# Performance work log

Hardware: AMD Instinct MI355X
Metric: run time of the kernel (lower is better)

## Reference

```python
import jax, jax.numpy as jnp
import numpy as np

LMAX = 4
S2_DIM = (LMAX + 1) ** 2                                  # 25: s2 irreps, mul 1 per l
SO3_DIM = sum((2 * l + 1) ** 2 for l in range(LMAX + 1))  # 165: so3 irreps, mul 2l+1 per l
B = 2048
F_S2, F_SO3 = 1, 16
N_S2_KERNEL = 48      # s2_healpix_grid(rec_level=1)
N_SO3_KERNEL = 192    # so3_near_identity_grid()
N_ACT_GRID = 4000     # SO3Activation resolution=10, aspect_ratio=2 -> 20x10x20, flattened
N_EVAL = 4608         # so3_healpix_grid(rec_level=2): 192 pixels x 24 gamma


def setup_inputs() -> dict:
    ks = jax.random.split(jax.random.key(0), 7)
    return {
        "x": jax.random.normal(ks[0], (B, F_S2, S2_DIM), jnp.float32),
        "w_s2": jax.random.normal(ks[1], (F_S2, F_SO3, N_S2_KERNEL), jnp.float32),
        "Y": jax.random.normal(ks[2], (N_S2_KERNEL, S2_DIM), jnp.float32),
        "w_so3": jax.random.normal(ks[3], (F_SO3, 1, N_SO3_KERNEL), jnp.float32),
        "D_kernel": jax.random.normal(ks[4], (N_SO3_KERNEL, SO3_DIM), jnp.float32),
        "D_act": jax.random.normal(ks[5], (N_ACT_GRID, SO3_DIM), jnp.float32),
        "eval_wigners": jax.random.normal(ks[6], (SO3_DIM, N_EVAL), jnp.float32) / np.sqrt(SO3_DIM),
    }


def _s2_to_so3_linear(x, psi):
    # e3nn o3.Linear(s2_irreps -> so3_irreps, f_in, f_out, external weights)
    # x:   [B, f_in, 25]  (mul 1 per degree l)
    # psi: [f_in, f_out, 25] ; column l^2+j is the weight to output-multiplicity j of degree l
    f_in, f_out = psi.shape[0], psi.shape[1]
    out, s = [], 0
    for l in range(LMAX + 1):
        d = 2 * l + 1
        x_l = x[..., s:s + d]                       # [B, f_in, d]
        p_l = psi[..., s:s + d]                     # [f_in, f_out, d] (j = out-mul idx)
        o = jnp.einsum('bxm,xyj->byjm', x_l, p_l) / np.sqrt(f_in)
        out.append(o.reshape(x.shape[0], f_out, d * d))
        s += d
    return jnp.concatenate(out, axis=-1)            # [B, f_out, 165]


def _so3_to_so3_linear(x, psi):
    # e3nn o3.Linear(so3_irreps -> so3_irreps, f_in, f_out, external weights)
    # x:   [B, f_in, 165] ; psi: [f_in, f_out, 165]
    f_in, f_out = psi.shape[0], psi.shape[1]
    out, s = [], 0
    for l in range(LMAX + 1):
        d = 2 * l + 1
        x_l = x[..., s:s + d * d].reshape(x.shape[0], f_in, d, d)   # [B,f_in,u,m]
        p_l = psi[..., s:s + d * d].reshape(f_in, f_out, d, d)      # [f_in,f_out,u,v]
        o = jnp.einsum('bxum,xyuv->byvm', x_l, p_l) / np.sqrt(f_in * d)
        out.append(o.reshape(x.shape[0], f_out, d * d))
        s += d * d
    return jnp.concatenate(out, axis=-1)            # [B, f_out, 165]


def _forward(x, w_s2, Y, w_so3, D_kernel, D_act, eval_wigners):
    # --- S2Convolution: kernel = SH-transform of grid weights, then irrep-wise linear
    psi1 = jnp.einsum('ni,xyn->xyi', Y, w_s2) / np.sqrt(N_S2_KERNEL)     # [1,16,25]
    h = _s2_to_so3_linear(x, psi1)                                        # [B,16,165]
    # --- SO3Activation: Fourier -> SO(3) grid -> relu -> Fourier
    g = jnp.einsum('bfi,gi->bfg', h, D_act) / np.sqrt(SO3_DIM)            # [B,16,4000]
    g = jax.nn.relu(g)
    h = jnp.einsum('bfg,gi->bfi', g, D_act) * (np.sqrt(SO3_DIM) / N_ACT_GRID)
    # --- SO3Convolution
    psi2 = jnp.einsum('ni,xyn->xyi', D_kernel, w_so3) / np.sqrt(N_SO3_KERNEL)  # [16,1,165]
    harmonics = _so3_to_so3_linear(h, psi2)                               # [B,1,165]
    # --- compute_probabilities: matmul with eval Wigner-D basis + softmax over grid
    probs = jax.nn.softmax(jnp.einsum('bfi,ie->be', harmonics, eval_wigners), axis=1)  # [B,4608]
    # --- top-k masking: zero out everything below the 5th-highest prob of sample 0
    fifth = jax.lax.top_k(probs, 5)[0][0, 4]
    probs = jnp.where(probs < fifth, 0.0, probs)
    return harmonics, probs


def reference(x, w_s2, Y, w_so3, D_kernel, D_act, eval_wigners):
    return _forward(x, w_s2, Y, w_so3, D_kernel, D_act, eval_wigners)
```

## Files before the change

kernel.cpp:

```cpp
#include <hip/hip_runtime.h>

typedef short bf16x8 __attribute__((ext_vector_type(8)));
typedef float f32x16 __attribute__((ext_vector_type(16)));
typedef int   i32x4  __attribute__((ext_vector_type(4)));

#define INV_SQRT165 0.07784989441615349f
#define FINAL_SCALE 0.0032113081446662823f
#define ZERO16 ((f32x16){0.f,0.f,0.f,0.f,0.f,0.f,0.f,0.f,0.f,0.f,0.f,0.f,0.f,0.f,0.f,0.f})

__device__ __forceinline__ unsigned short f2bf(float f) {
  unsigned int u = __builtin_bit_cast(unsigned int, f);
  unsigned int r = (u + 0x7FFFu + ((u >> 16) & 1u)) >> 16;
  return (unsigned short)r;
}
__device__ __forceinline__ float bf2f(unsigned short h) {
  unsigned int u = ((unsigned int)h) << 16;
  return __builtin_bit_cast(float, u);
}
__device__ __forceinline__ unsigned int pack_bf2(float lo, float hi) {
  return ((unsigned int)f2bf(hi) << 16) | (unsigned int)f2bf(lo);
}

__device__ __forceinline__ void gl_lds16(const void* g, void* l) {
  __builtin_amdgcn_global_load_lds(
      (const __attribute__((address_space(1))) unsigned int*)(unsigned long long)g,
      (__attribute__((address_space(3))) unsigned int*)(unsigned int)(unsigned long long)l,
      16, 0, 0);
}

__device__ __forceinline__ void decode_i(int i, int& lv, int& rel) {
  if (i < 1)       { lv = 0; rel = i; }
  else if (i < 10) { lv = 1; rel = i - 1; }
  else if (i < 35) { lv = 2; rel = i - 10; }
  else if (i < 84) { lv = 3; rel = i - 35; }
  else             { lv = 4; rel = i - 84; }
}
__device__ __forceinline__ int divq(int rel, int lv) {
  const int mag[5] = {32768, 10923, 6554, 4682, 3641};
  return (rel * mag[lv]) >> 15;
}

__global__ void psi_k(const float* __restrict__ Y, const float* __restrict__ w_s2,
                      const float* __restrict__ Dk, const float* __restrict__ w_so3,
                      float* __restrict__ psi1, float* __restrict__ psi2) {
  int bx = blockIdx.x;
  if (bx < 2) {
    int t = bx * 256 + threadIdx.x;
    if (t >= 400) return;
    int y = t / 25, i = t % 25;
    float s = 0.f;
    for (int n = 0; n < 48; n++) s += Y[n * 25 + i] * w_s2[y * 48 + n];
    psi1[t] = s * 0.14433756729740643f;
  } else {
    int t = (bx - 2) * 256 + threadIdx.x;
    if (t >= 2640) return;
    int ch = t / 165, i = t % 165;
    float s = 0.f;
    for (int n = 0; n < 192; n++) s += Dk[n * 165 + i] * w_so3[ch * 192 + n];
    psi2[t] = s * 0.07216878364870323f;
  }
}

__global__ __launch_bounds__(256) void prep_k(const float* __restrict__ Da,
                                              const float* __restrict__ ew,
                                              const float* __restrict__ psi1,
                                              unsigned short* __restrict__ e1pre,
                                              unsigned short* __restrict__ d2pre,
                                              unsigned short* __restrict__ ewpre) {
  __shared__ __align__(16) unsigned short lds[13824];
  const int tid = threadIdx.x;
  const int l = tid & 63, hl = l >> 5, ln = l & 31;
  if (blockIdx.x < 128) {
    const int ci = blockIdx.x, g0 = ci * 32;
    float* psi1L = (float*)(lds + 6464);
    for (int e = tid; e < 6400; e += 256) lds[e] = 0;
    for (int e = tid; e < 400; e += 256) psi1L[e] = psi1[e];
    __syncthreads();
    int rows = 4000 - g0; if (rows > 32) rows = 32; if (rows < 0) rows = 0;
    int ne = rows * 165;
    for (int e = tid; e < ne; e += 256) {
      int gl_ = e / 165, k = e - gl_ * 165;
      lds[gl_ * 200 + k] = f2bf(Da[g0 * 165 + e]);
    }
    __syncthreads();
#pragma unroll
    for (int it = 0; it < 3; it++) {
      int tt = it * 4 + (tid >> 6);
      int nf = tt >> 1, gk = tt & 1;
      unsigned short v[8];
#pragma unroll
      for (int j = 0; j < 8; j++)
        v[j] = lds[(gk * 16 + hl * 8 + j) * 200 + nf * 32 + ln];
      *(i32x4*)(d2pre + ci * 6144 + tt * 512 + l * 8) = *(i32x4*)v;
    }
    for (int yy = 0; yy < 16; yy++) {
#pragma unroll
      for (int it = 0; it < 4; it++) {
        int idx = it * 256 + tid;
        int kf = idx >> 9, r2 = idx & 511;
        int ll = r2 >> 3, j = r2 & 7;
        int lnn = ll & 31, hll = ll >> 5;
        int k = kf * 16 + hll * 8 + j;
        unsigned short ov = 0;
        if (k < 25) {
          int lv = (k < 1) ? 0 : (k < 4) ? 1 : (k < 9) ? 2 : (k < 16) ? 3 : 4;
          int d = 2 * lv + 1;
          int m = k - lv * lv;
          int off165 = lv * (4 * lv * lv - 1) / 3;
          float s = 0.f;
          const float* pr = psi1L + yy * 25 + lv * lv;
          const unsigned short* dr = lds + lnn * 200 + off165 + m;
          for (int j2 = 0; j2 < d; j2++) s += pr[j2] * bf2f(dr[j2 * d]);
          ov = f2bf(s);
        }
        e1pre[((yy * 128 + ci) * 2 + kf) * 512 + ll * 8 + j] = ov;
      }
    }
  } else {
    const int bx2 = blockIdx.x - 128;
    const int n0 = bx2 * 64;
    for (int e = tid; e < 13824; e += 256) lds[e] = 0;
    __syncthreads();
    for (int e = tid; e < 10560; e += 256) {
      int k = e >> 6, n = e & 63;
      lds[k * 72 + n] = f2bf(ew[k * 4608 + n0 + n]);
    }
    __syncthreads();
#pragma unroll
    for (int it = 0; it < 6; it++) {
      int tb = it * 4 + (tid >> 6);
      int nt2 = tb / 12, kf = tb - nt2 * 12;
      unsigned short v[8];
#pragma unroll
      for (int j = 0; j < 8; j++)
        v[j] = lds[(kf * 16 + hl * 8 + j) * 72 + nt2 * 32 + ln];
      *(i32x4*)(ewpre + (bx2 * 2 + nt2) * 6144 + kf * 512 + l * 8) = *(i32x4*)v;
    }
  }
}

__global__ __launch_bounds__(256, 2) void fused_mlp_k(
    const float* __restrict__ x,
    const unsigned short* __restrict__ e1pre,
    const unsigned short* __restrict__ d2pre,
    unsigned short* __restrict__ part)
{
  __shared__ __align__(16) unsigned char smem[28672];
  const int tid = threadIdx.x;
  const int w = tid >> 6, l = tid & 63;
  const int hl = l >> 5, ln = l & 31;
  const int h = blockIdx.x & 1;
  const int y = (blockIdx.x >> 1) & 15;
  const int btg = blockIdx.x >> 5;
  const int bt = btg * 4 + w;
  const int c0 = h * 64;

  bf16x8 xf[2];
  {
    const float* xr = x + (bt * 32 + ln) * 25;
#pragma unroll
    for (int kf = 0; kf < 2; kf++) {
      unsigned short v[8];
#pragma unroll
      for (int j = 0; j < 8; j++) {
        int k = kf * 16 + hl * 8 + j;
        v[j] = (k < 25) ? f2bf(xr[k]) : (unsigned short)0;
      }
      xf[kf] = *(bf16x8*)v;
    }
  }

  f32x16 o[6];
#pragma unroll
  for (int nf = 0; nf < 6; nf++) o[nf] = ZERO16;

  const unsigned short* ebase = e1pre + (y * 128) * 1024;

#pragma unroll
  for (int i = 0; i < 4; i++) {
    int tb = w * 4 + i;
    if (tb < 14) {
      const unsigned short* g = (tb < 12) ? (d2pre + c0 * 6144 + tb * 512 + l * 8)
                                          : (ebase + (c0 * 2 + (tb - 12)) * 512 + l * 8);
      gl_lds16(g, smem + tb * 1024);
    }
  }

  for (int ci = 0; ci < 64; ci++) {
    __syncthreads();
    const unsigned char* cb = smem + (ci & 1) * 14336;
    if (ci < 63) {
      const unsigned char* nb = smem + ((ci + 1) & 1) * 14336;
      const int c = c0 + ci + 1;
#pragma unroll
      for (int i = 0; i < 4; i++) {
        int tb = w * 4 + i;
        if (tb < 14) {
          const unsigned short* g = (tb < 12) ? (d2pre + c * 6144 + tb * 512 + l * 8)
                                              : (ebase + (c * 2 + (tb - 12)) * 512 + l * 8);
          gl_lds16(g, (void*)(nb + tb * 1024));
        }
      }
    }
    f32x16 c0a = ZERO16;
    {
      bf16x8 aE0 = *(const bf16x8*)(cb + 12288 + l * 16);
      bf16x8 aE1 = *(const bf16x8*)(cb + 13312 + l * 16);
      c0a = __builtin_amdgcn_mfma_f32_32x32x16_bf16(aE0, xf[0], c0a, 0, 0, 0);
      c0a = __builtin_amdgcn_mfma_f32_32x32x16_bf16(aE1, xf[1], c0a, 0, 0, 0);
    }
    unsigned int dw[8];
#pragma unroll
    for (int p = 0; p < 8; p++) {
      float v0 = fmaxf(c0a[2 * p]     * INV_SQRT165, 0.f);
      float v1 = fmaxf(c0a[2 * p + 1] * INV_SQRT165, 0.f);
      dw[p] = pack_bf2(v0, v1);
    }
    unsigned int r1 = __shfl_xor(hl ? dw[0] : dw[2], 32);
    unsigned int r2 = __shfl_xor(hl ? dw[1] : dw[3], 32);
    unsigned int r3 = __shfl_xor(hl ? dw[4] : dw[6], 32);
    unsigned int r4 = __shfl_xor(hl ? dw[5] : dw[7], 32);
    i32x4 a2i0, a2i1;
    if (hl == 0) {
      a2i0 = (i32x4){(int)dw[0], (int)dw[1], (int)r1, (int)r2};
      a2i1 = (i32x4){(int)dw[4], (int)dw[5], (int)r3, (int)r4};
    } else {
      a2i0 = (i32x4){(int)r1, (int)r2, (int)dw[2], (int)dw[3]};
      a2i1 = (i32x4){(int)r3, (int)r4, (int)dw[6], (int)dw[7]};
    }
    bf16x8 a2_0 = __builtin_bit_cast(bf16x8, a2i0);
    bf16x8 a2_1 = __builtin_bit_cast(bf16x8, a2i1);
#pragma unroll
    for (int gk = 0; gk < 2; gk++) {
      bf16x8 a2 = gk ? a2_1 : a2_0;
#pragma unroll
      for (int nf = 0; nf < 6; nf++) {
        bf16x8 b2 = *(const bf16x8*)(cb + (nf * 2 + gk) * 1024 + l * 16);
        o[nf] = __builtin_amdgcn_mfma_f32_32x32x16_bf16(a2, b2, o[nf], 0, 0, 0);
      }
    }
  }

  unsigned short* pp = part + (size_t)(h * 16 + y) * 2048 * 192 + bt * 32 * 192;
#pragma unroll
  for (int nf = 0; nf < 6; nf++) {
    int n = nf * 32 + ln;
    if (n < 176) {
#pragma unroll
      for (int r = 0; r < 16; r++) {
        int row = (r & 3) + 8 * (r >> 2) + 4 * hl;
        pp[row * 192 + n] = f2bf(o[nf][r]);
      }
    }
  }
}

__global__ __launch_bounds__(256) void so3_k(const unsigned short* __restrict__ part,
                                             const float* __restrict__ psi2,
                                             float* __restrict__ harm_out,
                                             unsigned short* __restrict__ harmbpre) {
  __shared__ float lds[4 * 16 * 180];
  const int tid = threadIdx.x;
  const int b0 = blockIdx.x * 4;
  {
    const int ybl = tid >> 2;
    const int yy = ybl & 15, bloc = ybl >> 4;
    const int s = tid & 3;
    const unsigned int* r0 = (const unsigned int*)(part + ((size_t)(0 * 16 + yy) * 2048 + b0 + bloc) * 192);
    const unsigned int* r1 = (const unsigned int*)(part + ((size_t)(1 * 16 + yy) * 2048 + b0 + bloc) * 192);
    float* dst = lds + (bloc * 16 + yy) * 180;
#pragma unroll
    for (int t = 0; t < 22; t++) {
      int d = s * 22 + t;
      if (d < 88) {
        unsigned int u0 = r0[d], u1 = r1[d];
        int n0 = d * 2;
        float lo = bf2f((unsigned short)(u0 & 0xFFFF)) + bf2f((unsigned short)(u1 & 0xFFFF));
        float hi = bf2f((unsigned short)(u0 >> 16))    + bf2f((unsigned short)(u1 >> 16));
        dst[n0]     = lo * FINAL_SCALE;
        dst[n0 + 1] = hi * FINAL_SCALE;
      }
    }
  }
  __syncthreads();
  for (int jj = tid; jj < 768; jj += 256) {
    int e = (jj * 683) >> 17;
    int i = jj - e * 192;
    int bb = b0 + e;
    unsigned short* hb = harmbpre + (((bb >> 5) * 12 + (i >> 4)) << 9)
                       + ((i >> 3) & 1) * 256 + (bb & 31) * 8 + (i & 7);
    if (i < 165) {
      const float* row0 = lds + e * (16 * 180);
      int lv, rel; decode_i(i, lv, rel);
      int d = 2 * lv + 1;
      int off = i - rel;
      int v = divq(rel, lv), m = rel - v * d;
      float s = 0.f;
      for (int ch = 0; ch < 16; ch++) {
        const float* rw = row0 + ch * 180 + off;
        const float* p2 = psi2 + ch * 165 + off;
        for (int u = 0; u < d; u++) s += rw[u * d + m] * p2[u * d + v];
      }
      s *= 0.25f * rsqrtf((float)d);
      harm_out[bb * 165 + i] = s;
      *hb = f2bf(s);
    } else {
      *hb = 0;
    }
  }
}

__global__ __launch_bounds__(64) void eval_k(
    const unsigned short* __restrict__ harmbpre,
    const unsigned short* __restrict__ ewpre,
    float* __restrict__ logits)
{
  const int l = threadIdx.x;
  const int hl = l >> 5, ln = l & 31;
  const int mt = blockIdx.y;
  const int n0 = blockIdx.x * 192;

  bf16x8 a[12];
  const short* ap = (const short*)harmbpre + mt * 6144 + l * 8;
#pragma unroll
  for (int kf = 0; kf < 12; kf++) a[kf] = *(const bf16x8*)(ap + kf * 512);

  f32x16 acc[6];
#pragma unroll
  for (int nf = 0; nf < 6; nf++) acc[nf] = ZERO16;

  const short* bp = (const short*)ewpre + (blockIdx.x * 6) * 6144 + l * 8;
#pragma unroll
  for (int kf = 0; kf < 12; kf++) {
#pragma unroll
    for (int nf = 0; nf < 6; nf++) {
      bf16x8 b = *(const bf16x8*)(bp + nf * 6144 + kf * 512);
      acc[nf] = __builtin_amdgcn_mfma_f32_32x32x16_bf16(a[kf], b, acc[nf], 0, 0, 0);
    }
  }
#pragma unroll
  for (int nf = 0; nf < 6; nf++) {
    const int col = n0 + nf * 32 + ln;
#pragma unroll
    for (int r = 0; r < 16; r++) {
      int row = (r & 3) + 8 * (r >> 2) + 4 * hl;
      logits[(mt * 32 + row) * 4608 + col] = acc[nf][r];
    }
  }
}

__global__ __launch_bounds__(256) void fifth_k(const float* __restrict__ logit0,
                                               float* __restrict__ fifth) {
  __shared__ float buf[4608];
  __shared__ float sm[4], ss[4];
  __shared__ float wv[4]; __shared__ int wi[4];
  __shared__ float gbest;
  const int tid = threadIdx.x;
  const int l = tid & 63, w = tid >> 6;
  float v[18];
  float mx = -3.4e38f;
#pragma unroll
  for (int i = 0; i < 18; i++) {
    v[i] = logit0[i * 256 + tid];
    buf[i * 256 + tid] = v[i];
    mx = fmaxf(mx, v[i]);
  }
#pragma unroll
  for (int off = 32; off >= 1; off >>= 1) mx = fmaxf(mx, __shfl_xor(mx, off));
  if (l == 0) sm[w] = mx;
  __syncthreads();
  mx = fmaxf(fmaxf(sm[0], sm[1]), fmaxf(sm[2], sm[3]));
  float s = 0.f;
#pragma unroll
  for (int i = 0; i < 18; i++) { v[i] = __expf(v[i] - mx); s += v[i]; }
#pragma unroll
  for (int off = 32; off >= 1; off >>= 1) s += __shfl_xor(s, off);
  if (l == 0) ss[w] = s;
  __syncthreads();
  s = ss[0] + ss[1] + ss[2] + ss[3];
  float inv = 1.f / s;

  float ff = 0.f;
  for (int it = 0; it < 5; it++) {
    float bm = -3.4e38f; int bi = 0;
    for (int i = tid; i < 4608; i += 256) {
      float xx = buf[i];
      if (xx > bm) { bm = xx; bi = i; }
    }
    for (int off = 32; off >= 1; off >>= 1) {
      float ov = __shfl_xor(bm, off); int oi = __shfl_xor(bi, off);
      if (ov > bm) { bm = ov; bi = oi; }
    }
    if (l == 0) { wv[w] = bm; wi[w] = bi; }
    __syncthreads();
    if (tid == 0) {
      float B = wv[0]; int I = wi[0];
      for (int k = 1; k < 4; k++) if (wv[k] > B) { B = wv[k]; I = wi[k]; }
      gbest = B;
      buf[I] = -3.4e38f;
    }
    __syncthreads();
    ff = gbest;
    __syncthreads();
  }
  if (tid == 0) *fifth = __expf(ff - mx) * inv;
}

__global__ __launch_bounds__(256) void smthresh_k(float* __restrict__ probs,
                                                  const float* __restrict__ fifth) {
  float* p = probs + (size_t)blockIdx.x * 4608;
  const int tid = threadIdx.x;
  const int l = tid & 63, w = tid >> 6;
  __shared__ float sm[4], ss[4];
  float v[18];
  float mx = -3.4e38f;
#pragma unroll
  for (int i = 0; i < 18; i++) { v[i] = p[i * 256 + tid]; mx = fmaxf(mx, v[i]); }
#pragma unroll
  for (int off = 32; off >= 1; off >>= 1) mx = fmaxf(mx, __shfl_xor(mx, off));
  if (l == 0) sm[w] = mx;
  __syncthreads();
  mx = fmaxf(fmaxf(sm[0], sm[1]), fmaxf(sm[2], sm[3]));
  float s = 0.f;
#pragma unroll
  for (int i = 0; i < 18; i++) { v[i] = __expf(v[i] - mx); s += v[i]; }
#pragma unroll
  for (int off = 32; off >= 1; off >>= 1) s += __shfl_xor(s, off);
  if (l == 0) ss[w] = s;
  __syncthreads();
  s = ss[0] + ss[1] + ss[2] + ss[3];
  float inv = 1.f / s;
  float t = *fifth;
#pragma unroll
  for (int i = 0; i < 18; i++) {
    float pv = v[i] * inv;
    p[i * 256 + tid] = (pv < t) ? 0.f : pv;
  }
}

extern "C" void kernel_launch(void* const* d_in, const int* in_sizes, int n_in,
                              void* d_out, int out_size, void* d_ws, size_t ws_size,
                              hipStream_t stream) {
  const float* x     = (const float*)d_in[0];
  const float* w_s2  = (const float*)d_in[1];
  const float* Y     = (const float*)d_in[2];
  const float* w_so3 = (const float*)d_in[3];
  const float* Dk    = (const float*)d_in[4];
  const float* Da    = (const float*)d_in[5];
  const float* ew    = (const float*)d_in[6];

  float* out = (float*)d_out;
  float* harm_out = out;
  float* probs    = out + 337920;
  unsigned short* part = (unsigned short*)probs;

  char* ws = (char*)d_ws;
  float* psi1  = (float*)(ws + 0);
  float* psi2  = (float*)(ws + 1600);
  float* fifth = (float*)(ws + 12160);
  unsigned short* e1pre    = (unsigned short*)(ws + 12288);
  unsigned short* d2pre    = (unsigned short*)(ws + 4206592);
  unsigned short* ewpre    = (unsigned short*)(ws + 5779456);
  unsigned short* harmbpre = (unsigned short*)(ws + 7548928);

  psi_k <<<13,  256, 0, stream>>>(Y, w_s2, Dk, w_so3, psi1, psi2);
  prep_k<<<200, 256, 0, stream>>>(Da, ew, psi1, e1pre, d2pre, ewpre);
  fused_mlp_k<<<512, 256, 0, stream>>>(x, e1pre, d2pre, part);
  so3_k<<<512, 256, 0, stream>>>(part, psi2, harm_out, harmbpre);
  eval_k<<<dim3(24, 64), 64, 0, stream>>>(harmbpre, ewpre, probs);
  fifth_k<<<1, 256, 0, stream>>>(probs, fifth);
  smthresh_k<<<2048, 256, 0, stream>>>(probs, fifth);
}
```

Before: 250.8 us.

## Fold psi kernel into prep, fold scales into weights, and retile MLP warps

Removes the separate psi_k launch: each prep block recomputes psi1 into shared memory, and extra blocks compute psi2. The 1/sqrt(165) scale moves into the e1 weights and the final scale into psi2, which drops per-element multiplies from the fused MLP and so3 kernels. In fused_mlp_k each warp now processes two 32-row batch tiles against half of the output columns, so every B fragment read from LDS is reused twice. The bf16 pack uses the HIP intrinsic. The cost is redundant psi1 recomputation across 128 blocks and changed register pressure in the MLP kernel.

```diff
diff --git a/kernel.cpp b/kernel.cpp
--- a/kernel.cpp
+++ b/kernel.cpp
@@ -1,4 +1,5 @@
 #include <hip/hip_runtime.h>
+#include <hip/hip_bf16.h>
 
 typedef short bf16x8 __attribute__((ext_vector_type(8)));
 typedef float f32x16 __attribute__((ext_vector_type(16)));
@@ -18,7 +19,10 @@
   return __builtin_bit_cast(float, u);
 }
 __device__ __forceinline__ unsigned int pack_bf2(float lo, float hi) {
-  return ((unsigned int)f2bf(hi) << 16) | (unsigned int)f2bf(lo);
+  __hip_bfloat162 r = __float22bfloat162_rn(make_float2(lo, hi));
+  unsigned int u;
+  __builtin_memcpy(&u, &r, 4);
+  return u;
 }
 
 __device__ __forceinline__ void gl_lds16(const void* g, void* l) {
@@ -40,33 +44,16 @@
   return (rel * mag[lv]) >> 15;
 }
 
-__global__ void psi_k(const float* __restrict__ Y, const float* __restrict__ w_s2,
-                      const float* __restrict__ Dk, const float* __restrict__ w_so3,
-                      float* __restrict__ psi1, float* __restrict__ psi2) {
-  int bx = blockIdx.x;
-  if (bx < 2) {
-    int t = bx * 256 + threadIdx.x;
-    if (t >= 400) return;
-    int y = t / 25, i = t % 25;
-    float s = 0.f;
-    for (int n = 0; n < 48; n++) s += Y[n * 25 + i] * w_s2[y * 48 + n];
-    psi1[t] = s * 0.14433756729740643f;
-  } else {
-    int t = (bx - 2) * 256 + threadIdx.x;
-    if (t >= 2640) return;
-    int ch = t / 165, i = t % 165;
-    float s = 0.f;
-    for (int n = 0; n < 192; n++) s += Dk[n * 165 + i] * w_so3[ch * 192 + n];
-    psi2[t] = s * 0.07216878364870323f;
-  }
-}
-
 __global__ __launch_bounds__(256) void prep_k(const float* __restrict__ Da,
                                               const float* __restrict__ ew,
-                                              const float* __restrict__ psi1,
+                                              const float* __restrict__ Y,
+                                              const float* __restrict__ w_s2,
+                                              const float* __restrict__ Dk,
+                                              const float* __restrict__ w_so3,
                                               unsigned short* __restrict__ e1pre,
                                               unsigned short* __restrict__ d2pre,
-                                              unsigned short* __restrict__ ewpre) {
+                                              unsigned short* __restrict__ ewpre,
+                                              float* __restrict__ psi2) {
   __shared__ __align__(16) unsigned short lds[13824];
   const int tid = threadIdx.x;
   const int l = tid & 63, hl = l >> 5, ln = l & 31;
@@ -74,7 +61,12 @@
     const int ci = blockIdx.x, g0 = ci * 32;
     float* psi1L = (float*)(lds + 6464);
     for (int e = tid; e < 6400; e += 256) lds[e] = 0;
-    for (int e = tid; e < 400; e += 256) psi1L[e] = psi1[e];
+    for (int e = tid; e < 400; e += 256) {
+      int yv = e / 25, iv = e % 25;
+      float s = 0.f;
+      for (int n = 0; n < 48; n++) s += Y[n * 25 + iv] * w_s2[yv * 48 + n];
+      psi1L[e] = s * 0.14433756729740643f;
+    }
     __syncthreads();
     int rows = 4000 - g0; if (rows > 32) rows = 32; if (rows < 0) rows = 0;
     int ne = rows * 165;
@@ -111,12 +103,12 @@
           const float* pr = psi1L + yy * 25 + lv * lv;
           const unsigned short* dr = lds + lnn * 200 + off165 + m;
           for (int j2 = 0; j2 < d; j2++) s += pr[j2] * bf2f(dr[j2 * d]);
-          ov = f2bf(s);
+          ov = f2bf(s * INV_SQRT165);
         }
         e1pre[((yy * 128 + ci) * 2 + kf) * 512 + ll * 8 + j] = ov;
       }
     }
-  } else {
+  } else if (blockIdx.x < 200) {
     const int bx2 = blockIdx.x - 128;
     const int n0 = bx2 * 64;
     for (int e = tid; e < 13824; e += 256) lds[e] = 0;
@@ -135,6 +127,14 @@
       for (int j = 0; j < 8; j++)
         v[j] = lds[(kf * 16 + hl * 8 + j) * 72 + nt2 * 32 + ln];
       *(i32x4*)(ewpre + (bx2 * 2 + nt2) * 6144 + kf * 512 + l * 8) = *(i32x4*)v;
+    }
+  } else {
+    int t = (blockIdx.x - 200) * 256 + tid;
+    if (t < 2640) {
+      int ch = t / 165, i = t % 165;
+      float s = 0.f;
+      for (int n = 0; n < 192; n++) s += Dk[n * 165 + i] * w_so3[ch * 192 + n];
+      psi2[t] = s * (0.07216878364870323f * FINAL_SCALE);
     }
   }
 }
@@ -151,13 +151,14 @@
   const int hl = l >> 5, ln = l & 31;
   const int h = blockIdx.x & 1;
   const int y = (blockIdx.x >> 1) & 15;
-  const int btg = blockIdx.x >> 5;
-  const int bt = btg * 4 + w;
+  const int bblk = blockIdx.x >> 5;
+  const int bw = w >> 1, ng = w & 1;
   const int c0 = h * 64;
 
-  bf16x8 xf[2];
-  {
-    const float* xr = x + (bt * 32 + ln) * 25;
+  bf16x8 xf[2][2];
+#pragma unroll
+  for (int t = 0; t < 2; t++) {
+    const float* xr = x + (bblk * 128 + bw * 64 + t * 32 + ln) * 25;
 #pragma unroll
     for (int kf = 0; kf < 2; kf++) {
       unsigned short v[8];
@@ -166,13 +167,13 @@
         int k = kf * 16 + hl * 8 + j;
         v[j] = (k < 25) ? f2bf(xr[k]) : (unsigned short)0;
       }
-      xf[kf] = *(bf16x8*)v;
+      xf[t][kf] = *(bf16x8*)v;
     }
   }
 
   f32x16 o[6];
 #pragma unroll
-  for (int nf = 0; nf < 6; nf++) o[nf] = ZERO16;
+  for (int i = 0; i < 6; i++) o[i] = ZERO16;
 
   const unsigned short* ebase = e1pre + (y * 128) * 1024;
 
@@ -202,54 +203,62 @@
         }
       }
     }
-    f32x16 c0a = ZERO16;
-    {
-      bf16x8 aE0 = *(const bf16x8*)(cb + 12288 + l * 16);
-      bf16x8 aE1 = *(const bf16x8*)(cb + 13312 + l * 16);
-      c0a = __builtin_amdgcn_mfma_f32_32x32x16_bf16(aE0, xf[0], c0a, 0, 0, 0);
-      c0a = __builtin_amdgcn_mfma_f32_32x32x16_bf16(aE1, xf[1], c0a, 0, 0, 0);
-    }
-    unsigned int dw[8];
-#pragma unroll
-    for (int p = 0; p < 8; p++) {
-      float v0 = fmaxf(c0a[2 * p]     * INV_SQRT165, 0.f);
-      float v1 = fmaxf(c0a[2 * p + 1] * INV_SQRT165, 0.f);
-      dw[p] = pack_bf2(v0, v1);
-    }
-    unsigned int r1 = __shfl_xor(hl ? dw[0] : dw[2], 32);
-    unsigned int r2 = __shfl_xor(hl ? dw[1] : dw[3], 32);
-    unsigned int r3 = __shfl_xor(hl ? dw[4] : dw[6], 32);
-    unsigned int r4 = __shfl_xor(hl ? dw[5] : dw[7], 32);
-    i32x4 a2i0, a2i1;
-    if (hl == 0) {
-      a2i0 = (i32x4){(int)dw[0], (int)dw[1], (int)r1, (int)r2};
-      a2i1 = (i32x4){(int)dw[4], (int)dw[5], (int)r3, (int)r4};
-    } else {
-      a2i0 = (i32x4){(int)r1, (int)r2, (int)dw[2], (int)dw[3]};
-      a2i1 = (i32x4){(int)r3, (int)r4, (int)dw[6], (int)dw[7]};
-    }
-    bf16x8 a2_0 = __builtin_bit_cast(bf16x8, a2i0);
-    bf16x8 a2_1 = __builtin_bit_cast(bf16x8, a2i1);
+    bf16x8 aE0 = *(const bf16x8*)(cb + 12288 + l * 16);
+    bf16x8 aE1 = *(const bf16x8*)(cb + 13312 + l * 16);
+    f32x16 s0 = ZERO16, s1 = ZERO16;
+    s0 = __builtin_amdgcn_mfma_f32_32x32x16_bf16(aE0, xf[0][0], s0, 0, 0, 0);
+    s1 = __builtin_amdgcn_mfma_f32_32x32x16_bf16(aE0, xf[1][0], s1, 0, 0, 0);
+    s0 = __builtin_amdgcn_mfma_f32_32x32x16_bf16(aE1, xf[0][1], s0, 0, 0, 0);
+    s1 = __builtin_amdgcn_mfma_f32_32x32x16_bf16(aE1, xf[1][1], s1, 0, 0, 0);
+
+    bf16x8 a2[2][2];
+#pragma unroll
+    for (int t = 0; t < 2; t++) {
+      const f32x16& sv = t ? s1 : s0;
+      unsigned int dw[8];
+#pragma unroll
+      for (int p = 0; p < 8; p++)
+        dw[p] = pack_bf2(fmaxf(sv[2 * p], 0.f), fmaxf(sv[2 * p + 1], 0.f));
+      unsigned int r1 = __shfl_xor(hl ? dw[0] : dw[2], 32);
+      unsigned int r2 = __shfl_xor(hl ? dw[1] : dw[3], 32);
+      unsigned int r3 = __shfl_xor(hl ? dw[4] : dw[6], 32);
+      unsigned int r4 = __shfl_xor(hl ? dw[5] : dw[7], 32);
+      i32x4 a2i0, a2i1;
+      if (hl == 0) {
+        a2i0 = (i32x4){(int)dw[0], (int)dw[1], (int)r1, (int)r2};
+        a2i1 = (i32x4){(int)dw[4], (int)dw[5], (int)r3, (int)r4};
+      } else {
+        a2i0 = (i32x4){(int)r1, (int)r2, (int)dw[2], (int)dw[3]};
+        a2i1 = (i32x4){(int)r3, (int)r4, (int)dw[6], (int)dw[7]};
+      }
+      a2[t][0] = __builtin_bit_cast(bf16x8, a2i0);
+      a2[t][1] = __builtin_bit_cast(bf16x8, a2i1);
+    }
+
+    const unsigned char* bbase = cb + ng * 6144;
 #pragma unroll
     for (int gk = 0; gk < 2; gk++) {
-      bf16x8 a2 = gk ? a2_1 : a2_0;
-#pragma unroll
-      for (int nf = 0; nf < 6; nf++) {
-        bf16x8 b2 = *(const bf16x8*)(cb + (nf * 2 + gk) * 1024 + l * 16);
-        o[nf] = __builtin_amdgcn_mfma_f32_32x32x16_bf16(a2, b2, o[nf], 0, 0, 0);
-      }
-    }
-  }
-
-  unsigned short* pp = part + (size_t)(h * 16 + y) * 2048 * 192 + bt * 32 * 192;
-#pragma unroll
-  for (int nf = 0; nf < 6; nf++) {
-    int n = nf * 32 + ln;
-    if (n < 176) {
-#pragma unroll
-      for (int r = 0; r < 16; r++) {
-        int row = (r & 3) + 8 * (r >> 2) + 4 * hl;
-        pp[row * 192 + n] = f2bf(o[nf][r]);
+#pragma unroll
+      for (int nf = 0; nf < 3; nf++) {
+        bf16x8 b2 = *(const bf16x8*)(bbase + (nf * 2 + gk) * 1024 + l * 16);
+        o[nf]     = __builtin_amdgcn_mfma_f32_32x32x16_bf16(a2[0][gk], b2, o[nf],     0, 0, 0);
+        o[3 + nf] = __builtin_amdgcn_mfma_f32_32x32x16_bf16(a2[1][gk], b2, o[3 + nf], 0, 0, 0);
+      }
+    }
+  }
+
+#pragma unroll
+  for (int t = 0; t < 2; t++) {
+    unsigned short* pp = part + (size_t)((h * 16 + y) * 2048 + bblk * 128 + bw * 64 + t * 32) * 192;
+#pragma unroll
+    for (int nf = 0; nf < 3; nf++) {
+      int n = ng * 96 + nf * 32 + ln;
+      if (n < 176) {
+#pragma unroll
+        for (int r = 0; r < 16; r++) {
+          int row = (r & 3) + 8 * (r >> 2) + 4 * hl;
+          pp[row * 192 + n] = f2bf(o[t * 3 + nf][r]);
+        }
       }
     }
   }
@@ -275,10 +284,8 @@
       if (d < 88) {
         unsigned int u0 = r0[d], u1 = r1[d];
         int n0 = d * 2;
-        float lo = bf2f((unsigned short)(u0 & 0xFFFF)) + bf2f((unsigned short)(u1 & 0xFFFF));
-        float hi = bf2f((unsigned short)(u0 >> 16))    + bf2f((unsigned short)(u1 >> 16));
-        dst[n0]     = lo * FINAL_SCALE;
-        dst[n0 + 1] = hi * FINAL_SCALE;
+        dst[n0]     = bf2f((unsigned short)(u0 & 0xFFFF)) + bf2f((unsigned short)(u1 & 0xFFFF));
+        dst[n0 + 1] = bf2f((unsigned short)(u0 >> 16))    + bf2f((unsigned short)(u1 >> 16));
       }
     }
   }
@@ -455,16 +462,14 @@
   unsigned short* part = (unsigned short*)probs;
 
   char* ws = (char*)d_ws;
-  float* psi1  = (float*)(ws + 0);
-  float* psi2  = (float*)(ws + 1600);
-  float* fifth = (float*)(ws + 12160);
+  float* psi2  = (float*)(ws + 0);
+  float* fifth = (float*)(ws + 10560);
   unsigned short* e1pre    = (unsigned short*)(ws + 12288);
   unsigned short* d2pre    = (unsigned short*)(ws + 4206592);
   unsigned short* ewpre    = (unsigned short*)(ws + 5779456);
   unsigned short* harmbpre = (unsigned short*)(ws + 7548928);
 
-  psi_k <<<13,  256, 0, stream>>>(Y, w_s2, Dk, w_so3, psi1, psi2);
-  prep_k<<<200, 256, 0, stream>>>(Da, ew, psi1, e1pre, d2pre, ewpre);
+  prep_k<<<211, 256, 0, stream>>>(Da, ew, Y, w_s2, Dk, w_so3, e1pre, d2pre, ewpre, psi2);
   fused_mlp_k<<<512, 256, 0, stream>>>(x, e1pre, d2pre, part);
   so3_k<<<512, 256, 0, stream>>>(part, psi2, harm_out, harmbpre);
   eval_k<<<dim3(24, 64), 64, 0, stream>>>(harmbpre, ewpre, probs);
```

After: 259.5 us. 1.03x slower.
